# Optimization experiments

Hardware: AMD Instinct MI355X
Metric: run time of the kernel (lower is better)

## Reference

```python
import jax, jax.numpy as jnp
import numpy as np

T, H, F, E, K = 1024, 2048, 1024, 8, 2  # tokens, hidden, intermediate, experts, top_k
RENORMALIZE = True


def setup_inputs() -> dict:
    key = jax.random.key(0)
    k1, k2, k3, k4, k5 = jax.random.split(key, 5)
    hidden_states = jax.random.normal(k1, (T, H), dtype=jnp.float32)
    router_logits = jax.random.normal(k2, (T, E), dtype=jnp.float32)
    w1 = jax.random.normal(k3, (E, H, F), dtype=jnp.float32) * 0.02  # gate proj
    w3 = jax.random.normal(k4, (E, H, F), dtype=jnp.float32) * 0.02  # up proj
    w2 = jax.random.normal(k5, (E, F, H), dtype=jnp.float32) * 0.02  # down proj
    return {"hidden_states": hidden_states, "router_logits": router_logits,
            "w1": w1, "w3": w3, "w2": w2}


def _moe_forward(x, router_logits, w1, w3, w2):
    # Top-K routing: softmax over all experts, select top-k, optional renormalize.
    probs = jax.nn.softmax(router_logits, axis=-1)            # [T, E]
    topk_vals, topk_ids = jax.lax.top_k(probs, K)             # [T, K]
    if RENORMALIZE:
        topk_vals = topk_vals / jnp.sum(topk_vals, axis=-1, keepdims=True)
    # Dense combine weights: zero for non-selected experts.   [T, E]
    tok_idx = jnp.arange(x.shape[0])[:, None]
    combine = jnp.zeros(probs.shape, dtype=x.dtype).at[tok_idx, topk_ids].set(topk_vals)
    # Expert SwiGLU FFN computed per expert over all tokens, masked-combined.
    g = jnp.einsum('th,ehf->etf', x, w1)                      # gate  [E, T, F]
    u = jnp.einsum('th,ehf->etf', x, w3)                      # up    [E, T, F]
    a = jax.nn.silu(g) * u                                    # silu activation
    y = jnp.einsum('etf,efh->eth', a, w2)                     # down  [E, T, H]
    out = jnp.einsum('eth,te->th', y, combine)                # weighted combine
    return out


def reference(hidden_states, router_logits, w1, w3, w2):
    return _moe_forward(hidden_states, router_logits, w1, w3, w2)
```

## Files before the change

kernel.cpp:

```cpp
#include <hip/hip_runtime.h>
#include <cstdint>
#include <cstddef>

#define T_TOK 1024
#define H_DIM 2048
#define F_DIM 1024
#define E_EXP 8
#define BM 64
#define BN 64
#define BK 64
#define SP 70
#define MAX_TILES 40
#define ROWCAP 2560

#define I_COUNTS 0
#define I_CURSOR 8
#define I_OFFS   16
#define I_NTILES 25
#define I_TILE_E 32
#define I_TILE_R0 80
#define I_TOPKID 128
#define I_TOPKW  2176
#define I_ROWTOK 4224
#define I_ROWW   6784
#define B_XB     37888
#define B_AWS    (37888 + T_TOK*H_DIM*2)

typedef __bf16 bf16x8 __attribute__((ext_vector_type(8)));
typedef __bf16 bf16x4 __attribute__((ext_vector_type(4)));
typedef float  f32x4  __attribute__((ext_vector_type(4)));

#define MFMA(a,b,c) __builtin_amdgcn_mfma_f32_16x16x32_bf16(a,b,c,0,0,0)

__global__ __launch_bounds__(256) void k_router(const float* __restrict__ logits,
                                                int* __restrict__ ws_i) {
  int t = blockIdx.x * 256 + threadIdx.x;
  if (t >= T_TOK) return;
  float l[E_EXP];
#pragma unroll
  for (int e = 0; e < E_EXP; ++e) l[e] = logits[t * E_EXP + e];
  int b0 = 0; float v0 = l[0];
#pragma unroll
  for (int e = 1; e < E_EXP; ++e) if (l[e] > v0) { v0 = l[e]; b0 = e; }
  int b1 = -1; float v1 = -3.4e38f;
#pragma unroll
  for (int e = 0; e < E_EXP; ++e) if (e != b0 && l[e] > v1) { v1 = l[e]; b1 = e; }
  float w0 = 1.f / (1.f + __expf(v1 - v0));
  ws_i[I_TOPKID + t * 2 + 0] = b0;
  ws_i[I_TOPKID + t * 2 + 1] = b1;
  float* ws_f = (float*)ws_i;
  ws_f[I_TOPKW + t * 2 + 0] = w0;
  ws_f[I_TOPKW + t * 2 + 1] = 1.f - w0;
  atomicAdd(&ws_i[I_COUNTS + b0], 1);
  atomicAdd(&ws_i[I_COUNTS + b1], 1);
}

__global__ __launch_bounds__(256) void k_scan(int* __restrict__ ws_i) {
  if (threadIdx.x == 0) {
    int off = 0, nt = 0;
    for (int e = 0; e < E_EXP; ++e) {
      ws_i[I_OFFS + e] = off;
      int c = ws_i[I_COUNTS + e];
      int ntile = (c + BM - 1) / BM;
      for (int i = 0; i < ntile; ++i) {
        ws_i[I_TILE_E + nt] = e;
        ws_i[I_TILE_R0 + nt] = off + i * BM;
        ++nt;
      }
      off += ntile * BM;
      ws_i[I_CURSOR + e] = 0;
    }
    ws_i[I_OFFS + 8] = off;
    ws_i[I_NTILES] = nt;
  }
  __syncthreads();
  for (int i = threadIdx.x; i < ROWCAP; i += 256) ws_i[I_ROWTOK + i] = -1;
}

__global__ __launch_bounds__(256) void k_assign(int* __restrict__ ws_i) {
  int t = blockIdx.x * 256 + threadIdx.x;
  if (t >= T_TOK) return;
  float* ws_f = (float*)ws_i;
#pragma unroll
  for (int k = 0; k < 2; ++k) {
    int e = ws_i[I_TOPKID + t * 2 + k];
    int p = atomicAdd(&ws_i[I_CURSOR + e], 1);
    int s = ws_i[I_OFFS + e] + p;
    ws_i[I_ROWTOK + s] = t;
    ws_f[I_ROWW + s] = ws_f[I_TOPKW + t * 2 + k];
  }
}

__global__ __launch_bounds__(256) void k_cvt(const float* __restrict__ x,
                                             __bf16* __restrict__ xb) {
  long i = (long)(blockIdx.x * 256 + threadIdx.x) * 8;
  float4 a = *(const float4*)(x + i);
  float4 b = *(const float4*)(x + i + 4);
  bf16x8 v;
  v[0] = (__bf16)a.x; v[1] = (__bf16)a.y; v[2] = (__bf16)a.z; v[3] = (__bf16)a.w;
  v[4] = (__bf16)b.x; v[5] = (__bf16)b.y; v[6] = (__bf16)b.z; v[7] = (__bf16)b.w;
  *(bf16x8*)(xb + i) = v;
}

__global__ __launch_bounds__(256) void k_gemm1(const __bf16* __restrict__ xb,
                                               const float* __restrict__ w1,
                                               const float* __restrict__ w3,
                                               const int* __restrict__ ws_i,
                                               __bf16* __restrict__ aws) {
  __shared__ __bf16 As[BM][SP];
  __shared__ __bf16 B1s[BN][SP];
  __shared__ __bf16 B3s[BN][SP];
  __shared__ int s_tok[BM];
  const int p = blockIdx.x;
  const int lg = (p & 7) * 80 + (p >> 3);
  const int tile = lg % MAX_TILES;
  const int n0 = (lg / MAX_TILES) * BN;
  if (tile >= ws_i[I_NTILES]) return;
  const int e  = ws_i[I_TILE_E + tile];
  const int r0 = ws_i[I_TILE_R0 + tile];
  const int tid = threadIdx.x, lane = tid & 63, wid = tid >> 6;
  const int wm = wid >> 1, wn = wid & 1;
  const int l15 = lane & 15, lk8 = (lane >> 4) << 3;
  const int ar = tid >> 3, ac = (tid & 7) * 8;
  const int nb = (tid & 15) * 4, kq = (tid >> 4) * 4;
  if (tid < BM) {
    int tk = ws_i[I_ROWTOK + r0 + tid];
    s_tok[tid] = tk < 0 ? 0 : tk;
  }
  __syncthreads();
  const int tok0 = s_tok[ar], tok1 = s_tok[ar + 32];
  const __bf16* xA0 = xb + (size_t)tok0 * H_DIM + ac;
  const __bf16* xA1 = xb + (size_t)tok1 * H_DIM + ac;
  const float* pB1 = w1 + (size_t)e * H_DIM * F_DIM + n0 + nb + (size_t)kq * F_DIM;
  const float* pB3 = w3 + (size_t)e * H_DIM * F_DIM + n0 + nb + (size_t)kq * F_DIM;

  bf16x8 rA0, rA1;
  f32x4 q1[4], q3[4];

  auto LOADG = [&](int K0) {
    rA0 = *(const bf16x8*)(xA0 + K0);
    rA1 = *(const bf16x8*)(xA1 + K0);
#pragma unroll
    for (int j = 0; j < 4; ++j) {
      q1[j] = *(const f32x4*)(pB1 + (size_t)(K0 + j) * F_DIM);
      q3[j] = *(const f32x4*)(pB3 + (size_t)(K0 + j) * F_DIM);
    }
  };
  auto WRITEL = [&]() {
    *(bf16x8*)&As[ar][ac] = rA0;
    *(bf16x8*)&As[ar + 32][ac] = rA1;
#pragma unroll
    for (int u = 0; u < 4; ++u) {
      bf16x4 v1, v3;
#pragma unroll
      for (int j = 0; j < 4; ++j) { v1[j] = (__bf16)q1[j][u]; v3[j] = (__bf16)q3[j][u]; }
      *(bf16x4*)&B1s[nb + u][kq] = v1;
      *(bf16x4*)&B3s[nb + u][kq] = v3;
    }
  };

  f32x4 accg[2][2] = {}; f32x4 accu[2][2] = {};
  LOADG(0);
  for (int k0 = 0; k0 < H_DIM; k0 += BK) {
    if (k0) __syncthreads();
    WRITEL();
    if (k0 + BK < H_DIM) LOADG(k0 + BK);
    __syncthreads();
#pragma unroll
    for (int kk = 0; kk < 2; ++kk) {
      const int kb = kk * 32 + lk8;
      bf16x8 a0  = *(const bf16x8*)&As[wm * 32 + l15][kb];
      bf16x8 a1  = *(const bf16x8*)&As[wm * 32 + 16 + l15][kb];
      bf16x8 b10 = *(const bf16x8*)&B1s[wn * 32 + l15][kb];
      bf16x8 b11 = *(const bf16x8*)&B1s[wn * 32 + 16 + l15][kb];
      bf16x8 b30 = *(const bf16x8*)&B3s[wn * 32 + l15][kb];
      bf16x8 b31 = *(const bf16x8*)&B3s[wn * 32 + 16 + l15][kb];
      accg[0][0] = MFMA(a0, b10, accg[0][0]);
      accg[0][1] = MFMA(a0, b11, accg[0][1]);
      accg[1][0] = MFMA(a1, b10, accg[1][0]);
      accg[1][1] = MFMA(a1, b11, accg[1][1]);
      accu[0][0] = MFMA(a0, b30, accu[0][0]);
      accu[0][1] = MFMA(a0, b31, accu[0][1]);
      accu[1][0] = MFMA(a1, b30, accu[1][0]);
      accu[1][1] = MFMA(a1, b31, accu[1][1]);
    }
  }
#pragma unroll
  for (int fm = 0; fm < 2; ++fm)
#pragma unroll
    for (int fn = 0; fn < 2; ++fn)
#pragma unroll
      for (int r = 0; r < 4; ++r) {
        float g = accg[fm][fn][r], u = accu[fm][fn][r];
        float a = g / (1.f + __expf(-g)) * u;
        int row = r0 + wm * 32 + fm * 16 + ((lane >> 4) << 2) + r;
        int col = n0 + wn * 32 + fn * 16 + l15;
        aws[(size_t)row * F_DIM + col] = (__bf16)a;
      }
}

__global__ __launch_bounds__(256) void k_gemm2(const __bf16* __restrict__ aws,
                                               const float* __restrict__ w2,
                                               const int* __restrict__ ws_i,
                                               float* __restrict__ out) {
  __shared__ __bf16 As[BM][SP];
  __shared__ __bf16 Bs[BN][SP];
  __shared__ int s_tok[BM];
  __shared__ float s_w[BM];
  const int p = blockIdx.x;
  const int lg = (p & 7) * 160 + (p >> 3);
  const int tile = lg % MAX_TILES;
  const int h0 = (lg / MAX_TILES) * BN;
  if (tile >= ws_i[I_NTILES]) return;
  const int e  = ws_i[I_TILE_E + tile];
  const int r0 = ws_i[I_TILE_R0 + tile];
  const int tid = threadIdx.x, lane = tid & 63, wid = tid >> 6;
  const int wm = wid >> 1, wn = wid & 1;
  const int l15 = lane & 15, lk8 = (lane >> 4) << 3;
  const int ar = tid >> 3, ac = (tid & 7) * 8;
  const int nb = (tid & 15) * 4, kq = (tid >> 4) * 4;
  const float* ws_f = (const float*)ws_i;
  if (tid < BM) {
    s_tok[tid] = ws_i[I_ROWTOK + r0 + tid];
    s_w[tid]   = ws_f[I_ROWW + r0 + tid];
  }
  __syncthreads();
  const __bf16* pA0 = aws + (size_t)(r0 + ar) * F_DIM + ac;
  const __bf16* pA1 = aws + (size_t)(r0 + ar + 32) * F_DIM + ac;
  const float* pB2 = w2 + (size_t)e * F_DIM * H_DIM + h0 + nb + (size_t)kq * H_DIM;

  bf16x8 rA0, rA1;
  f32x4 q2[4];
  auto LOADG = [&](int K0) {
    rA0 = *(const bf16x8*)(pA0 + K0);
    rA1 = *(const bf16x8*)(pA1 + K0);
#pragma unroll
    for (int j = 0; j < 4; ++j) q2[j] = *(const f32x4*)(pB2 + (size_t)(K0 + j) * H_DIM);
  };
  auto WRITEL = [&]() {
    *(bf16x8*)&As[ar][ac] = rA0;
    *(bf16x8*)&As[ar + 32][ac] = rA1;
#pragma unroll
    for (int u = 0; u < 4; ++u) {
      bf16x4 v;
#pragma unroll
      for (int j = 0; j < 4; ++j) v[j] = (__bf16)q2[j][u];
      *(bf16x4*)&Bs[nb + u][kq] = v;
    }
  };

  f32x4 acc[2][2] = {};
  LOADG(0);
  for (int k0 = 0; k0 < F_DIM; k0 += BK) {
    if (k0) __syncthreads();
    WRITEL();
    if (k0 + BK < F_DIM) LOADG(k0 + BK);
    __syncthreads();
#pragma unroll
    for (int kk = 0; kk < 2; ++kk) {
      const int kb = kk * 32 + lk8;
      bf16x8 a0 = *(const bf16x8*)&As[wm * 32 + l15][kb];
      bf16x8 a1 = *(const bf16x8*)&As[wm * 32 + 16 + l15][kb];
      bf16x8 b0 = *(const bf16x8*)&Bs[wn * 32 + l15][kb];
      bf16x8 b1 = *(const bf16x8*)&Bs[wn * 32 + 16 + l15][kb];
      acc[0][0] = MFMA(a0, b0, acc[0][0]);
      acc[0][1] = MFMA(a0, b1, acc[0][1]);
      acc[1][0] = MFMA(a1, b0, acc[1][0]);
      acc[1][1] = MFMA(a1, b1, acc[1][1]);
    }
  }
#pragma unroll
  for (int fm = 0; fm < 2; ++fm)
#pragma unroll
    for (int fn = 0; fn < 2; ++fn)
#pragma unroll
      for (int r = 0; r < 4; ++r) {
        int lrow = wm * 32 + fm * 16 + ((lane >> 4) << 2) + r;
        int t = s_tok[lrow];
        if (t >= 0) {
          float v = acc[fm][fn][r] * s_w[lrow];
          atomicAdd(out + (size_t)t * H_DIM + h0 + wn * 32 + fn * 16 + l15, v);
        }
      }
}

extern "C" void kernel_launch(void* const* d_in, const int* in_sizes, int n_in,
                              void* d_out, int out_size, void* d_ws, size_t ws_size,
                              hipStream_t stream) {
  (void)in_sizes; (void)n_in; (void)out_size; (void)ws_size;
  const float* x      = (const float*)d_in[0];
  const float* logits = (const float*)d_in[1];
  const float* w1     = (const float*)d_in[2];
  const float* w3     = (const float*)d_in[3];
  const float* w2     = (const float*)d_in[4];
  float* out = (float*)d_out;
  int* ws_i = (int*)d_ws;
  __bf16* xb  = (__bf16*)((char*)d_ws + B_XB);
  __bf16* aws = (__bf16*)((char*)d_ws + B_AWS);

  hipMemsetAsync(d_ws, 0, 512, stream);
  hipMemsetAsync(d_out, 0, (size_t)T_TOK * H_DIM * sizeof(float), stream);

  k_router<<<dim3(T_TOK / 256), 256, 0, stream>>>(logits, ws_i);
  k_scan<<<1, 256, 0, stream>>>(ws_i);
  k_assign<<<dim3(T_TOK / 256), 256, 0, stream>>>(ws_i);
  k_cvt<<<dim3(T_TOK * H_DIM / (256 * 8)), 256, 0, stream>>>(x, xb);
  k_gemm1<<<dim3(MAX_TILES * (F_DIM / BN)), 256, 0, stream>>>(xb, w1, w3, ws_i, aws);
  k_gemm2<<<dim3(MAX_TILES * (H_DIM / BN)), 256, 0, stream>>>(aws, w2, ws_i, out);
}
```

Baseline: 137.3 us.

## Fuse routing kernels into one block and double-buffer GEMM global prefetch

```diff
diff --git a/kernel.cpp b/kernel.cpp
--- a/kernel.cpp
+++ b/kernel.cpp
@@ -13,14 +13,9 @@
 #define MAX_TILES 40
 #define ROWCAP 2560
 
-#define I_COUNTS 0
-#define I_CURSOR 8
-#define I_OFFS   16
 #define I_NTILES 25
 #define I_TILE_E 32
 #define I_TILE_R0 80
-#define I_TOPKID 128
-#define I_TOPKW  2176
 #define I_ROWTOK 4224
 #define I_ROWW   6784
 #define B_XB     37888
@@ -32,10 +27,13 @@
 
 #define MFMA(a,b,c) __builtin_amdgcn_mfma_f32_16x16x32_bf16(a,b,c,0,0,0)
 
-__global__ __launch_bounds__(256) void k_router(const float* __restrict__ logits,
+__global__ __launch_bounds__(1024) void k_route(const float* __restrict__ logits,
                                                 int* __restrict__ ws_i) {
-  int t = blockIdx.x * 256 + threadIdx.x;
-  if (t >= T_TOK) return;
+  __shared__ int cnt[E_EXP], cur[E_EXP], offs_s[E_EXP];
+  const int t = threadIdx.x;
+  float* ws_f = (float*)ws_i;
+  if (t < E_EXP) { cnt[t] = 0; cur[t] = 0; }
+  __syncthreads();
   float l[E_EXP];
 #pragma unroll
   for (int e = 0; e < E_EXP; ++e) l[e] = logits[t * E_EXP + e];
@@ -46,48 +44,37 @@
 #pragma unroll
   for (int e = 0; e < E_EXP; ++e) if (e != b0 && l[e] > v1) { v1 = l[e]; b1 = e; }
   float w0 = 1.f / (1.f + __expf(v1 - v0));
-  ws_i[I_TOPKID + t * 2 + 0] = b0;
-  ws_i[I_TOPKID + t * 2 + 1] = b1;
-  float* ws_f = (float*)ws_i;
-  ws_f[I_TOPKW + t * 2 + 0] = w0;
-  ws_f[I_TOPKW + t * 2 + 1] = 1.f - w0;
-  atomicAdd(&ws_i[I_COUNTS + b0], 1);
-  atomicAdd(&ws_i[I_COUNTS + b1], 1);
-}
-
-__global__ __launch_bounds__(256) void k_scan(int* __restrict__ ws_i) {
-  if (threadIdx.x == 0) {
+  float w1 = 1.f - w0;
+  atomicAdd(&cnt[b0], 1);
+  atomicAdd(&cnt[b1], 1);
+  __syncthreads();
+  if (t == 0) {
     int off = 0, nt = 0;
     for (int e = 0; e < E_EXP; ++e) {
-      ws_i[I_OFFS + e] = off;
-      int c = ws_i[I_COUNTS + e];
-      int ntile = (c + BM - 1) / BM;
+      offs_s[e] = off;
+      int ntile = (cnt[e] + BM - 1) / BM;
       for (int i = 0; i < ntile; ++i) {
         ws_i[I_TILE_E + nt] = e;
         ws_i[I_TILE_R0 + nt] = off + i * BM;
         ++nt;
       }
       off += ntile * BM;
-      ws_i[I_CURSOR + e] = 0;
     }
-    ws_i[I_OFFS + 8] = off;
     ws_i[I_NTILES] = nt;
   }
-  __syncthreads();
-  for (int i = threadIdx.x; i < ROWCAP; i += 256) ws_i[I_ROWTOK + i] = -1;
-}
-
-__global__ __launch_bounds__(256) void k_assign(int* __restrict__ ws_i) {
-  int t = blockIdx.x * 256 + threadIdx.x;
-  if (t >= T_TOK) return;
-  float* ws_f = (float*)ws_i;
-#pragma unroll
-  for (int k = 0; k < 2; ++k) {
-    int e = ws_i[I_TOPKID + t * 2 + k];
-    int p = atomicAdd(&ws_i[I_CURSOR + e], 1);
-    int s = ws_i[I_OFFS + e] + p;
+  for (int i = t; i < ROWCAP; i += 1024) ws_i[I_ROWTOK + i] = -1;
+  __syncthreads();
+  {
+    int p = atomicAdd(&cur[b0], 1);
+    int s = offs_s[b0] + p;
     ws_i[I_ROWTOK + s] = t;
-    ws_f[I_ROWW + s] = ws_f[I_TOPKW + t * 2 + k];
+    ws_f[I_ROWW + s] = w0;
+  }
+  {
+    int p = atomicAdd(&cur[b1], 1);
+    int s = offs_s[b1] + p;
+    ws_i[I_ROWTOK + s] = t;
+    ws_f[I_ROWW + s] = w1;
   }
 }
 
@@ -102,11 +89,32 @@
   *(bf16x8*)(xb + i) = v;
 }
 
-__global__ __launch_bounds__(256) void k_gemm1(const __bf16* __restrict__ xb,
-                                               const float* __restrict__ w1,
-                                               const float* __restrict__ w3,
-                                               const int* __restrict__ ws_i,
-                                               __bf16* __restrict__ aws) {
+#define LOADG1(S, K0) do { \
+  rA0_##S = *(const bf16x8*)(xA0 + (K0)); \
+  rA1_##S = *(const bf16x8*)(xA1 + (K0)); \
+  _Pragma("unroll") \
+  for (int j = 0; j < 4; ++j) { \
+    q1_##S[j] = *(const f32x4*)(pB1 + (size_t)((K0) + j) * F_DIM); \
+    q3_##S[j] = *(const f32x4*)(pB3 + (size_t)((K0) + j) * F_DIM); \
+  } } while (0)
+
+#define WRITEL1(S) do { \
+  *(bf16x8*)&As[ar][ac] = rA0_##S; \
+  *(bf16x8*)&As[ar + 32][ac] = rA1_##S; \
+  _Pragma("unroll") \
+  for (int u = 0; u < 4; ++u) { \
+    bf16x4 v1, v3; \
+    _Pragma("unroll") \
+    for (int j = 0; j < 4; ++j) { v1[j] = (__bf16)q1_##S[j][u]; v3[j] = (__bf16)q3_##S[j][u]; } \
+    *(bf16x4*)&B1s[nb + u][kq] = v1; \
+    *(bf16x4*)&B3s[nb + u][kq] = v3; \
+  } } while (0)
+
+__global__ __launch_bounds__(256, 4) void k_gemm1(const __bf16* __restrict__ xb,
+                                                  const float* __restrict__ w1,
+                                                  const float* __restrict__ w3,
+                                                  const int* __restrict__ ws_i,
+                                                  __bf16* __restrict__ aws) {
   __shared__ __bf16 As[BM][SP];
   __shared__ __bf16 B1s[BN][SP];
   __shared__ __bf16 B3s[BN][SP];
@@ -134,38 +142,11 @@
   const float* pB1 = w1 + (size_t)e * H_DIM * F_DIM + n0 + nb + (size_t)kq * F_DIM;
   const float* pB3 = w3 + (size_t)e * H_DIM * F_DIM + n0 + nb + (size_t)kq * F_DIM;
 
-  bf16x8 rA0, rA1;
-  f32x4 q1[4], q3[4];
-
-  auto LOADG = [&](int K0) {
-    rA0 = *(const bf16x8*)(xA0 + K0);
-    rA1 = *(const bf16x8*)(xA1 + K0);
-#pragma unroll
-    for (int j = 0; j < 4; ++j) {
-      q1[j] = *(const f32x4*)(pB1 + (size_t)(K0 + j) * F_DIM);
-      q3[j] = *(const f32x4*)(pB3 + (size_t)(K0 + j) * F_DIM);
-    }
-  };
-  auto WRITEL = [&]() {
-    *(bf16x8*)&As[ar][ac] = rA0;
-    *(bf16x8*)&As[ar + 32][ac] = rA1;
-#pragma unroll
-    for (int u = 0; u < 4; ++u) {
-      bf16x4 v1, v3;
-#pragma unroll
-      for (int j = 0; j < 4; ++j) { v1[j] = (__bf16)q1[j][u]; v3[j] = (__bf16)q3[j][u]; }
-      *(bf16x4*)&B1s[nb + u][kq] = v1;
-      *(bf16x4*)&B3s[nb + u][kq] = v3;
-    }
-  };
-
+  bf16x8 rA0_0, rA1_0, rA0_1, rA1_1;
+  f32x4 q1_0[4], q3_0[4], q1_1[4], q3_1[4];
   f32x4 accg[2][2] = {}; f32x4 accu[2][2] = {};
-  LOADG(0);
-  for (int k0 = 0; k0 < H_DIM; k0 += BK) {
-    if (k0) __syncthreads();
-    WRITEL();
-    if (k0 + BK < H_DIM) LOADG(k0 + BK);
-    __syncthreads();
+
+  auto COMPUTE = [&]() {
 #pragma unroll
     for (int kk = 0; kk < 2; ++kk) {
       const int kb = kk * 32 + lk8;
@@ -184,6 +165,21 @@
       accu[1][0] = MFMA(a1, b30, accu[1][0]);
       accu[1][1] = MFMA(a1, b31, accu[1][1]);
     }
+  };
+
+  LOADG1(0, 0);
+  LOADG1(1, BK);
+  for (int k0 = 0; k0 < H_DIM; k0 += 2 * BK) {
+    if (k0) __syncthreads();
+    WRITEL1(0);
+    if (k0 + 2 * BK < H_DIM) LOADG1(0, k0 + 2 * BK);
+    __syncthreads();
+    COMPUTE();
+    __syncthreads();
+    WRITEL1(1);
+    if (k0 + 3 * BK < H_DIM) LOADG1(1, k0 + 3 * BK);
+    __syncthreads();
+    COMPUTE();
   }
 #pragma unroll
   for (int fm = 0; fm < 2; ++fm)
@@ -199,10 +195,29 @@
       }
 }
 
-__global__ __launch_bounds__(256) void k_gemm2(const __bf16* __restrict__ aws,
-                                               const float* __restrict__ w2,
-                                               const int* __restrict__ ws_i,
-                                               float* __restrict__ out) {
+#define LOADG2(S, K0) do { \
+  rA0_##S = *(const bf16x8*)(pA0 + (K0)); \
+  rA1_##S = *(const bf16x8*)(pA1 + (K0)); \
+  _Pragma("unroll") \
+  for (int j = 0; j < 4; ++j) \
+    q2_##S[j] = *(const f32x4*)(pB2 + (size_t)((K0) + j) * H_DIM); \
+  } while (0)
+
+#define WRITEL2(S) do { \
+  *(bf16x8*)&As[ar][ac] = rA0_##S; \
+  *(bf16x8*)&As[ar + 32][ac] = rA1_##S; \
+  _Pragma("unroll") \
+  for (int u = 0; u < 4; ++u) { \
+    bf16x4 v; \
+    _Pragma("unroll") \
+    for (int j = 0; j < 4; ++j) v[j] = (__bf16)q2_##S[j][u]; \
+    *(bf16x4*)&Bs[nb + u][kq] = v; \
+  } } while (0)
+
+__global__ __launch_bounds__(256, 4) void k_gemm2(const __bf16* __restrict__ aws,
+                                                  const float* __restrict__ w2,
+                                                  const int* __restrict__ ws_i,
+                                                  float* __restrict__ out) {
   __shared__ __bf16 As[BM][SP];
   __shared__ __bf16 Bs[BN][SP];
   __shared__ int s_tok[BM];
@@ -229,33 +244,11 @@
   const __bf16* pA1 = aws + (size_t)(r0 + ar + 32) * F_DIM + ac;
   const float* pB2 = w2 + (size_t)e * F_DIM * H_DIM + h0 + nb + (size_t)kq * H_DIM;
 
-  bf16x8 rA0, rA1;
-  f32x4 q2[4];
-  auto LOADG = [&](int K0) {
-    rA0 = *(const bf16x8*)(pA0 + K0);
-    rA1 = *(const bf16x8*)(pA1 + K0);
-#pragma unroll
-    for (int j = 0; j < 4; ++j) q2[j] = *(const f32x4*)(pB2 + (size_t)(K0 + j) * H_DIM);
-  };
-  auto WRITEL = [&]() {
-    *(bf16x8*)&As[ar][ac] = rA0;
-    *(bf16x8*)&As[ar + 32][ac] = rA1;
-#pragma unroll
-    for (int u = 0; u < 4; ++u) {
-      bf16x4 v;
-#pragma unroll
-      for (int j = 0; j < 4; ++j) v[j] = (__bf16)q2[j][u];
-      *(bf16x4*)&Bs[nb + u][kq] = v;
-    }
-  };
-
+  bf16x8 rA0_0, rA1_0, rA0_1, rA1_1;
+  f32x4 q2_0[4], q2_1[4];
   f32x4 acc[2][2] = {};
-  LOADG(0);
-  for (int k0 = 0; k0 < F_DIM; k0 += BK) {
-    if (k0) __syncthreads();
-    WRITEL();
-    if (k0 + BK < F_DIM) LOADG(k0 + BK);
-    __syncthreads();
+
+  auto COMPUTE = [&]() {
 #pragma unroll
     for (int kk = 0; kk < 2; ++kk) {
       const int kb = kk * 32 + lk8;
@@ -268,6 +261,21 @@
       acc[1][0] = MFMA(a1, b0, acc[1][0]);
       acc[1][1] = MFMA(a1, b1, acc[1][1]);
     }
+  };
+
+  LOADG2(0, 0);
+  LOADG2(1, BK);
+  for (int k0 = 0; k0 < F_DIM; k0 += 2 * BK) {
+    if (k0) __syncthreads();
+    WRITEL2(0);
+    if (k0 + 2 * BK < F_DIM) LOADG2(0, k0 + 2 * BK);
+    __syncthreads();
+    COMPUTE();
+    __syncthreads();
+    WRITEL2(1);
+    if (k0 + 3 * BK < F_DIM) LOADG2(1, k0 + 3 * BK);
+    __syncthreads();
+    COMPUTE();
   }
 #pragma unroll
   for (int fm = 0; fm < 2; ++fm)
@@ -298,13 +306,9 @@
   __bf16* xb  = (__bf16*)((char*)d_ws + B_XB);
   __bf16* aws = (__bf16*)((char*)d_ws + B_AWS);
 
-  hipMemsetAsync(d_ws, 0, 512, stream);
   hipMemsetAsync(d_out, 0, (size_t)T_TOK * H_DIM * sizeof(float), stream);
-
-  k_router<<<dim3(T_TOK / 256), 256, 0, stream>>>(logits, ws_i);
-  k_scan<<<1, 256, 0, stream>>>(ws_i);
-  k_assign<<<dim3(T_TOK / 256), 256, 0, stream>>>(ws_i);
   k_cvt<<<dim3(T_TOK * H_DIM / (256 * 8)), 256, 0, stream>>>(x, xb);
+  k_route<<<1, 1024, 0, stream>>>(logits, ws_i);
   k_gemm1<<<dim3(MAX_TILES * (F_DIM / BN)), 256, 0, stream>>>(xb, w1, w3, ws_i, aws);
   k_gemm2<<<dim3(MAX_TILES * (H_DIM / BN)), 256, 0, stream>>>(aws, w2, ws_i, out);
 }
```

Result: slower. 283.3 us (+106.3%).

## Fuse routing kernels into one block, narrow gemm1 tile, add MFMA priority hints

Applied to the files above, without the earlier changes.

```diff
diff --git a/kernel.cpp b/kernel.cpp
--- a/kernel.cpp
+++ b/kernel.cpp
@@ -7,20 +7,16 @@
 #define F_DIM 1024
 #define E_EXP 8
 #define BM 64
-#define BN 64
 #define BK 64
+#define BN1 32
+#define BN2 64
 #define SP 70
 #define MAX_TILES 40
 #define ROWCAP 2560
 
-#define I_COUNTS 0
-#define I_CURSOR 8
-#define I_OFFS   16
 #define I_NTILES 25
 #define I_TILE_E 32
 #define I_TILE_R0 80
-#define I_TOPKID 128
-#define I_TOPKW  2176
 #define I_ROWTOK 4224
 #define I_ROWW   6784
 #define B_XB     37888
@@ -28,14 +24,18 @@
 
 typedef __bf16 bf16x8 __attribute__((ext_vector_type(8)));
 typedef __bf16 bf16x4 __attribute__((ext_vector_type(4)));
+typedef __bf16 bf16x2 __attribute__((ext_vector_type(2)));
 typedef float  f32x4  __attribute__((ext_vector_type(4)));
 
 #define MFMA(a,b,c) __builtin_amdgcn_mfma_f32_16x16x32_bf16(a,b,c,0,0,0)
 
-__global__ __launch_bounds__(256) void k_router(const float* __restrict__ logits,
+__global__ __launch_bounds__(1024) void k_route(const float* __restrict__ logits,
                                                 int* __restrict__ ws_i) {
-  int t = blockIdx.x * 256 + threadIdx.x;
-  if (t >= T_TOK) return;
+  __shared__ int cnt[E_EXP], cur[E_EXP], offs_s[E_EXP];
+  const int t = threadIdx.x;
+  float* ws_f = (float*)ws_i;
+  if (t < E_EXP) { cnt[t] = 0; cur[t] = 0; }
+  __syncthreads();
   float l[E_EXP];
 #pragma unroll
   for (int e = 0; e < E_EXP; ++e) l[e] = logits[t * E_EXP + e];
@@ -46,48 +46,37 @@
 #pragma unroll
   for (int e = 0; e < E_EXP; ++e) if (e != b0 && l[e] > v1) { v1 = l[e]; b1 = e; }
   float w0 = 1.f / (1.f + __expf(v1 - v0));
-  ws_i[I_TOPKID + t * 2 + 0] = b0;
-  ws_i[I_TOPKID + t * 2 + 1] = b1;
-  float* ws_f = (float*)ws_i;
-  ws_f[I_TOPKW + t * 2 + 0] = w0;
-  ws_f[I_TOPKW + t * 2 + 1] = 1.f - w0;
-  atomicAdd(&ws_i[I_COUNTS + b0], 1);
-  atomicAdd(&ws_i[I_COUNTS + b1], 1);
-}
-
-__global__ __launch_bounds__(256) void k_scan(int* __restrict__ ws_i) {
-  if (threadIdx.x == 0) {
+  float w1 = 1.f - w0;
+  atomicAdd(&cnt[b0], 1);
+  atomicAdd(&cnt[b1], 1);
+  __syncthreads();
+  if (t == 0) {
     int off = 0, nt = 0;
     for (int e = 0; e < E_EXP; ++e) {
-      ws_i[I_OFFS + e] = off;
-      int c = ws_i[I_COUNTS + e];
-      int ntile = (c + BM - 1) / BM;
+      offs_s[e] = off;
+      int ntile = (cnt[e] + BM - 1) / BM;
       for (int i = 0; i < ntile; ++i) {
         ws_i[I_TILE_E + nt] = e;
         ws_i[I_TILE_R0 + nt] = off + i * BM;
         ++nt;
       }
       off += ntile * BM;
-      ws_i[I_CURSOR + e] = 0;
-    }
-    ws_i[I_OFFS + 8] = off;
+    }
     ws_i[I_NTILES] = nt;
   }
-  __syncthreads();
-  for (int i = threadIdx.x; i < ROWCAP; i += 256) ws_i[I_ROWTOK + i] = -1;
-}
-
-__global__ __launch_bounds__(256) void k_assign(int* __restrict__ ws_i) {
-  int t = blockIdx.x * 256 + threadIdx.x;
-  if (t >= T_TOK) return;
-  float* ws_f = (float*)ws_i;
-#pragma unroll
-  for (int k = 0; k < 2; ++k) {
-    int e = ws_i[I_TOPKID + t * 2 + k];
-    int p = atomicAdd(&ws_i[I_CURSOR + e], 1);
-    int s = ws_i[I_OFFS + e] + p;
+  for (int i = t; i < ROWCAP; i += 1024) ws_i[I_ROWTOK + i] = -1;
+  __syncthreads();
+  {
+    int p = atomicAdd(&cur[b0], 1);
+    int s = offs_s[b0] + p;
     ws_i[I_ROWTOK + s] = t;
-    ws_f[I_ROWW + s] = ws_f[I_TOPKW + t * 2 + k];
+    ws_f[I_ROWW + s] = w0;
+  }
+  {
+    int p = atomicAdd(&cur[b1], 1);
+    int s = offs_s[b1] + p;
+    ws_i[I_ROWTOK + s] = t;
+    ws_f[I_ROWW + s] = w1;
   }
 }
 
@@ -108,21 +97,21 @@
                                                const int* __restrict__ ws_i,
                                                __bf16* __restrict__ aws) {
   __shared__ __bf16 As[BM][SP];
-  __shared__ __bf16 B1s[BN][SP];
-  __shared__ __bf16 B3s[BN][SP];
+  __shared__ __bf16 B1s[BN1][SP];
+  __shared__ __bf16 B3s[BN1][SP];
   __shared__ int s_tok[BM];
   const int p = blockIdx.x;
-  const int lg = (p & 7) * 80 + (p >> 3);
+  const int lg = (p & 7) * 160 + (p >> 3);
   const int tile = lg % MAX_TILES;
-  const int n0 = (lg / MAX_TILES) * BN;
+  const int n0 = (lg / MAX_TILES) * BN1;
   if (tile >= ws_i[I_NTILES]) return;
   const int e  = ws_i[I_TILE_E + tile];
   const int r0 = ws_i[I_TILE_R0 + tile];
   const int tid = threadIdx.x, lane = tid & 63, wid = tid >> 6;
-  const int wm = wid >> 1, wn = wid & 1;
+  const int wm = wid;
   const int l15 = lane & 15, lk8 = (lane >> 4) << 3;
   const int ar = tid >> 3, ac = (tid & 7) * 8;
-  const int nb = (tid & 15) * 4, kq = (tid >> 4) * 4;
+  const int nb = (tid & 7) * 4, kq = (tid >> 3) * 2;
   if (tid < BM) {
     int tk = ws_i[I_ROWTOK + r0 + tid];
     s_tok[tid] = tk < 0 ? 0 : tk;
@@ -135,13 +124,14 @@
   const float* pB3 = w3 + (size_t)e * H_DIM * F_DIM + n0 + nb + (size_t)kq * F_DIM;
 
   bf16x8 rA0, rA1;
-  f32x4 q1[4], q3[4];
+  f32x4 q1[2], q3[2];
+  f32x4 accg[2] = {}; f32x4 accu[2] = {};
 
   auto LOADG = [&](int K0) {
     rA0 = *(const bf16x8*)(xA0 + K0);
     rA1 = *(const bf16x8*)(xA1 + K0);
 #pragma unroll
-    for (int j = 0; j < 4; ++j) {
+    for (int j = 0; j < 2; ++j) {
       q1[j] = *(const f32x4*)(pB1 + (size_t)(K0 + j) * F_DIM);
       q3[j] = *(const f32x4*)(pB3 + (size_t)(K0 + j) * F_DIM);
     }
@@ -151,52 +141,46 @@
     *(bf16x8*)&As[ar + 32][ac] = rA1;
 #pragma unroll
     for (int u = 0; u < 4; ++u) {
-      bf16x4 v1, v3;
-#pragma unroll
-      for (int j = 0; j < 4; ++j) { v1[j] = (__bf16)q1[j][u]; v3[j] = (__bf16)q3[j][u]; }
-      *(bf16x4*)&B1s[nb + u][kq] = v1;
-      *(bf16x4*)&B3s[nb + u][kq] = v3;
-    }
-  };
-
-  f32x4 accg[2][2] = {}; f32x4 accu[2][2] = {};
+      bf16x2 v1, v3;
+      v1[0] = (__bf16)q1[0][u]; v1[1] = (__bf16)q1[1][u];
+      v3[0] = (__bf16)q3[0][u]; v3[1] = (__bf16)q3[1][u];
+      *(bf16x2*)&B1s[nb + u][kq] = v1;
+      *(bf16x2*)&B3s[nb + u][kq] = v3;
+    }
+  };
+
   LOADG(0);
   for (int k0 = 0; k0 < H_DIM; k0 += BK) {
     if (k0) __syncthreads();
     WRITEL();
     if (k0 + BK < H_DIM) LOADG(k0 + BK);
     __syncthreads();
+    __builtin_amdgcn_s_setprio(1);
 #pragma unroll
     for (int kk = 0; kk < 2; ++kk) {
       const int kb = kk * 32 + lk8;
-      bf16x8 a0  = *(const bf16x8*)&As[wm * 32 + l15][kb];
-      bf16x8 a1  = *(const bf16x8*)&As[wm * 32 + 16 + l15][kb];
-      bf16x8 b10 = *(const bf16x8*)&B1s[wn * 32 + l15][kb];
-      bf16x8 b11 = *(const bf16x8*)&B1s[wn * 32 + 16 + l15][kb];
-      bf16x8 b30 = *(const bf16x8*)&B3s[wn * 32 + l15][kb];
-      bf16x8 b31 = *(const bf16x8*)&B3s[wn * 32 + 16 + l15][kb];
-      accg[0][0] = MFMA(a0, b10, accg[0][0]);
-      accg[0][1] = MFMA(a0, b11, accg[0][1]);
-      accg[1][0] = MFMA(a1, b10, accg[1][0]);
-      accg[1][1] = MFMA(a1, b11, accg[1][1]);
-      accu[0][0] = MFMA(a0, b30, accu[0][0]);
-      accu[0][1] = MFMA(a0, b31, accu[0][1]);
-      accu[1][0] = MFMA(a1, b30, accu[1][0]);
-      accu[1][1] = MFMA(a1, b31, accu[1][1]);
-    }
-  }
-#pragma unroll
-  for (int fm = 0; fm < 2; ++fm)
-#pragma unroll
-    for (int fn = 0; fn < 2; ++fn)
-#pragma unroll
-      for (int r = 0; r < 4; ++r) {
-        float g = accg[fm][fn][r], u = accu[fm][fn][r];
-        float a = g / (1.f + __expf(-g)) * u;
-        int row = r0 + wm * 32 + fm * 16 + ((lane >> 4) << 2) + r;
-        int col = n0 + wn * 32 + fn * 16 + l15;
-        aws[(size_t)row * F_DIM + col] = (__bf16)a;
-      }
+      bf16x8 a   = *(const bf16x8*)&As[wm * 16 + l15][kb];
+      bf16x8 b10 = *(const bf16x8*)&B1s[l15][kb];
+      bf16x8 b11 = *(const bf16x8*)&B1s[16 + l15][kb];
+      bf16x8 b30 = *(const bf16x8*)&B3s[l15][kb];
+      bf16x8 b31 = *(const bf16x8*)&B3s[16 + l15][kb];
+      accg[0] = MFMA(a, b10, accg[0]);
+      accg[1] = MFMA(a, b11, accg[1]);
+      accu[0] = MFMA(a, b30, accu[0]);
+      accu[1] = MFMA(a, b31, accu[1]);
+    }
+    __builtin_amdgcn_s_setprio(0);
+  }
+#pragma unroll
+  for (int fn = 0; fn < 2; ++fn)
+#pragma unroll
+    for (int r = 0; r < 4; ++r) {
+      float g = accg[fn][r], u = accu[fn][r];
+      float a = g / (1.f + __expf(-g)) * u;
+      int row = r0 + wm * 16 + ((lane >> 4) << 2) + r;
+      int col = n0 + fn * 16 + l15;
+      aws[(size_t)row * F_DIM + col] = (__bf16)a;
+    }
 }
 
 __global__ __launch_bounds__(256) void k_gemm2(const __bf16* __restrict__ aws,
@@ -204,13 +188,13 @@
                                                const int* __restrict__ ws_i,
                                                float* __restrict__ out) {
   __shared__ __bf16 As[BM][SP];
-  __shared__ __bf16 Bs[BN][SP];
+  __shared__ __bf16 Bs[BN2][SP];
   __shared__ int s_tok[BM];
   __shared__ float s_w[BM];
   const int p = blockIdx.x;
   const int lg = (p & 7) * 160 + (p >> 3);
   const int tile = lg % MAX_TILES;
-  const int h0 = (lg / MAX_TILES) * BN;
+  const int h0 = (lg / MAX_TILES) * BN2;
   if (tile >= ws_i[I_NTILES]) return;
   const int e  = ws_i[I_TILE_E + tile];
   const int r0 = ws_i[I_TILE_R0 + tile];
@@ -242,10 +226,11 @@
     *(bf16x8*)&As[ar + 32][ac] = rA1;
 #pragma unroll
     for (int u = 0; u < 4; ++u) {
-      bf16x4 v;
-#pragma unroll
-      for (int j = 0; j < 4; ++j) v[j] = (__bf16)q2[j][u];
-      *(bf16x4*)&Bs[nb + u][kq] = v;
+      bf16x2 va, vb;
+      va[0] = (__bf16)q2[0][u]; va[1] = (__bf16)q2[1][u];
+      vb[0] = (__bf16)q2[2][u]; vb[1] = (__bf16)q2[3][u];
+      *(bf16x2*)&Bs[nb + u][kq] = va;
+      *(bf16x2*)&Bs[nb + u][kq + 2] = vb;
     }
   };
 
@@ -256,6 +241,7 @@
     WRITEL();
     if (k0 + BK < F_DIM) LOADG(k0 + BK);
     __syncthreads();
+    __builtin_amdgcn_s_setprio(1);
 #pragma unroll
     for (int kk = 0; kk < 2; ++kk) {
       const int kb = kk * 32 + lk8;
@@ -268,6 +254,7 @@
       acc[1][0] = MFMA(a1, b0, acc[1][0]);
       acc[1][1] = MFMA(a1, b1, acc[1][1]);
     }
+    __builtin_amdgcn_s_setprio(0);
   }
 #pragma unroll
   for (int fm = 0; fm < 2; ++fm)
@@ -298,13 +285,9 @@
   __bf16* xb  = (__bf16*)((char*)d_ws + B_XB);
   __bf16* aws = (__bf16*)((char*)d_ws + B_AWS);
 
-  hipMemsetAsync(d_ws, 0, 512, stream);
   hipMemsetAsync(d_out, 0, (size_t)T_TOK * H_DIM * sizeof(float), stream);
-
-  k_router<<<dim3(T_TOK / 256), 256, 0, stream>>>(logits, ws_i);
-  k_scan<<<1, 256, 0, stream>>>(ws_i);
-  k_assign<<<dim3(T_TOK / 256), 256, 0, stream>>>(ws_i);
+  k_route<<<1, 1024, 0, stream>>>(logits, ws_i);
   k_cvt<<<dim3(T_TOK * H_DIM / (256 * 8)), 256, 0, stream>>>(x, xb);
-  k_gemm1<<<dim3(MAX_TILES * (F_DIM / BN)), 256, 0, stream>>>(xb, w1, w3, ws_i, aws);
-  k_gemm2<<<dim3(MAX_TILES * (H_DIM / BN)), 256, 0, stream>>>(aws, w2, ws_i, out);
-}
+  k_gemm1<<<dim3(MAX_TILES * (F_DIM / BN1)), 256, 0, stream>>>(xb, w1, w3, ws_i, aws);
+  k_gemm2<<<dim3(MAX_TILES * (H_DIM / BN2)), 256, 0, stream>>>(aws, w2, ws_i, out);
+}
```

Result: faster. 122.5 us (-10.8%).
